# Performance work log

Hardware: AMD Instinct MI355X
Metric: run time of the kernel (lower is better)

The kernel has to match this reference:

```python
import jax, jax.numpy as jnp
import numpy as np

# Dimensions (see shape_source):
B = 256    # number of nodes (atoms)
C = 64     # num_features (channels)
Y = 16     # spherical basis size: dims of 0e+1o+2e+3o = 1+3+5+7
Z = 23     # number of symmetric-contraction paths (U.size(-1))
E = 10     # n_node_attributes (number of chemical elements, one-hot)
CORR = 3   # correlation order -> spare dims 'wxv'
CG_DENSITY = 0.1  # CG coefficient tensors are highly sparse


def setup_inputs() -> dict:
    key = jax.random.key(0)
    kU, kM, kW, kZ, kA = jax.random.split(key, 5)
    # U buffer: shape (Y,)*CORR + (Y, Z) = (16,16,16,16,23), sparse like real CG coeffs
    U = jax.random.normal(kU, (Y,) * CORR + (Y, Z), dtype=jnp.float32)
    mask = jax.random.uniform(kM, U.shape) < CG_DENSITY
    U = U * mask.astype(jnp.float32)
    # W parameter: (n_node_attributes, Z, num_features), init randn/Z as in module
    W = jax.random.normal(kW, (E, Z, C), dtype=jnp.float32) / Z
    # node embeddings: (B, C, Y)  ('bci' in the einsum)
    node_embeddings = jax.random.normal(kZ, (B, C, Y), dtype=jnp.float32)
    # node attributes: one-hot element encodings (B, E)  ('be')
    elem = jax.random.randint(kA, (B,), 0, E)
    node_attributes = jax.nn.one_hot(elem, E, dtype=jnp.float32)
    return {
        "U": U,
        "W": W,
        "node_embeddings": node_embeddings,
        "node_attributes": node_attributes,
    }


def reference(U, W, node_embeddings, node_attributes):
    # Faithful to: torch.einsum('wxvik,ekc,bci,be->bcwxv', U, W, z, a)
    # Efficient contraction order (avoids any (B,*,Y^3) intermediate except the output):
    Wb = jnp.einsum('ekc,be->bkc', W, node_attributes)        # (B, Z, C): per-node path weights
    P = jnp.einsum('bkc,bci->bcik', Wb, node_embeddings)      # (B, C, Y, Z)
    out = jnp.einsum('wxvik,bcik->bcwxv', U, P)               # (B, C, Y, Y, Y)
    return out
```

## Files before the change

kernel.cpp:

```cpp
#include <hip/hip_runtime.h>
#include <hip/hip_bf16.h>

#define B_NODES 256
#define C_FEAT  64
#define Y_DIM   16
#define Z_PATH  23
#define E_ATTR  10
#define WXV     4096
#define K_REAL  368
#define K_PAD   384
#define M_DIM   16384
#define N_DIM   4096

typedef __attribute__((ext_vector_type(8))) short bf16x8;
typedef __attribute__((ext_vector_type(8))) unsigned short u16x8;
typedef __attribute__((ext_vector_type(4))) float f32x4;

__device__ inline unsigned short f2bf(float x) {
    union { float f; unsigned u; } v; v.f = x;
    unsigned r = v.u + 0x7fffu + ((v.u >> 16) & 1u);
    return (unsigned short)(r >> 16);
}

__device__ inline void gload_lds16(const void* g, void* l) {
    __builtin_amdgcn_global_load_lds(
        (const __attribute__((address_space(1))) void*)g,
        (__attribute__((address_space(3))) void*)l,
        16, 0, 0);
}

__global__ __launch_bounds__(256) void prep_combined(
    const float* __restrict__ U, const float* __restrict__ W,
    const float* __restrict__ z, const float* __restrict__ attr,
    unsigned short* __restrict__ A, unsigned short* __restrict__ Ub)
{
    int blk = blockIdx.x;
    int tid = threadIdx.x;
    if (blk < B_NODES) {
        int b = blk;
        __shared__ float t_lds[Z_PATH * C_FEAT];
        __shared__ float z_lds[C_FEAT * Y_DIM];
        __shared__ float a_lds[E_ATTR];
        if (tid < E_ATTR) a_lds[tid] = attr[b * E_ATTR + tid];
        ((float4*)z_lds)[tid] = ((const float4*)(z + (size_t)b * 1024))[tid];
        __syncthreads();
        for (int idx = tid; idx < Z_PATH * C_FEAT; idx += 256) {
            int k = idx >> 6;
            int c = idx & 63;
            float acc = 0.f;
            #pragma unroll
            for (int e = 0; e < E_ATTR; ++e)
                acc += a_lds[e] * W[(e * Z_PATH + k) * C_FEAT + c];
            t_lds[idx] = acc;
        }
        __syncthreads();
        unsigned short* Ab = A + (size_t)b * C_FEAT * K_PAD;
        for (int u = tid; u < C_FEAT * 48; u += 256) {
            int c = u / 48;
            int g = u - c * 48;
            int j0 = g * 8;
            u16x8 pack;
            #pragma unroll
            for (int jj = 0; jj < 8; ++jj) {
                int j = j0 + jj;
                float v = 0.f;
                if (j < K_REAL) {
                    int i = j / Z_PATH;
                    int k = j - i * Z_PATH;
                    v = z_lds[c * Y_DIM + i] * t_lds[k * C_FEAT + c];
                }
                pack[jj] = f2bf(v);
            }
            *(u16x8*)&Ab[c * K_PAD + j0] = pack;
        }
    } else {
        int f = (blk - B_NODES) * 256 + tid;
        int row = f / 96;
        int q = f - row * 96;
        int j = q * 4;
        unsigned short o[4] = {0, 0, 0, 0};
        if (j < K_REAL) {
            float4 v = *(const float4*)(U + (size_t)row * K_REAL + j);
            o[0] = f2bf(v.x); o[1] = f2bf(v.y); o[2] = f2bf(v.z); o[3] = f2bf(v.w);
        }
        unsigned short* dst = Ub + (size_t)row * K_PAD + j;
        dst[0] = o[0]; dst[1] = o[1]; dst[2] = o[2]; dst[3] = o[3];
    }
}

__global__ __launch_bounds__(256) void gemm_kernel(
    const unsigned short* __restrict__ A,
    const unsigned short* __restrict__ Bt,
    float* __restrict__ C)
{
    __shared__ unsigned short sA[2][128 * 32];
    __shared__ unsigned short sB[2][128 * 32];

    int bid = blockIdx.x;
    int wg = (bid & 7) * 512 + (bid >> 3);
    int tm = wg >> 5;
    int tn = wg & 31;
    int tid = threadIdx.x;
    int lane = tid & 63;
    int w = tid >> 6;
    int wm = w >> 1, wn = w & 1;

    f32x4 acc[4][4];
    #pragma unroll
    for (int p = 0; p < 4; ++p)
        #pragma unroll
        for (int q = 0; q < 4; ++q)
            acc[p][q] = (f32x4){0.f, 0.f, 0.f, 0.f};

    const char* gA = (const char*)A + (size_t)(tm * 128) * (K_PAD * 2);
    const char* gB = (const char*)Bt + (size_t)(tn * 128) * (K_PAD * 2);
    int ch0 = w * 2;
    int lrow = lane >> 2;
    int lk16 = (lane & 3) * 16;
    int fr_row = lane & 15;
    int fr_k = (lane >> 4) * 8;

    auto stage = [&](int t, int buf) {
        #pragma unroll
        for (int s = 0; s < 2; ++s) {
            int ch = ch0 + s;
            int r = ch * 16 + lrow;
            gload_lds16(gA + (size_t)r * (K_PAD * 2) + t * 64 + lk16,
                        (char*)&sA[buf][0] + ch * 1024);
            gload_lds16(gB + (size_t)r * (K_PAD * 2) + t * 64 + lk16,
                        (char*)&sB[buf][0] + ch * 1024);
        }
    };

    stage(0, 0);
    stage(1, 1);
    __builtin_amdgcn_sched_barrier(0);
    asm volatile("s_waitcnt vmcnt(4)" ::: "memory");
    __builtin_amdgcn_sched_barrier(0);
    __builtin_amdgcn_s_barrier();

    #pragma unroll
    for (int t = 0; t < 12; ++t) {
        const int cur = t & 1;
        bf16x8 af[4], bfr[4];
        #pragma unroll
        for (int fm = 0; fm < 4; ++fm)
            af[fm] = *(const bf16x8*)&sA[cur][(wm * 64 + fm * 16 + fr_row) * 32 + fr_k];
        #pragma unroll
        for (int fn = 0; fn < 4; ++fn)
            bfr[fn] = *(const bf16x8*)&sB[cur][(wn * 64 + fn * 16 + fr_row) * 32 + fr_k];
        #pragma unroll
        for (int fm = 0; fm < 4; ++fm)
            #pragma unroll
            for (int fn = 0; fn < 4; ++fn)
                acc[fm][fn] = __builtin_amdgcn_mfma_f32_16x16x32_bf16(
                    af[fm], bfr[fn], acc[fm][fn], 0, 0, 0);
        if (t < 11) {
            __builtin_amdgcn_sched_barrier(0);
            __builtin_amdgcn_s_barrier();
            if (t < 10) stage(t + 2, cur);
            __builtin_amdgcn_sched_barrier(0);
            if (t < 10) { asm volatile("s_waitcnt vmcnt(4)" ::: "memory"); }
            else        { asm volatile("s_waitcnt vmcnt(0)" ::: "memory"); }
            __builtin_amdgcn_sched_barrier(0);
            __builtin_amdgcn_s_barrier();
            __builtin_amdgcn_sched_barrier(0);
        }
    }

    int r0 = tm * 128 + wm * 64 + (lane >> 4) * 4;
    int c0 = tn * 128 + wn * 64 + (lane & 15);
    #pragma unroll
    for (int fm = 0; fm < 4; ++fm)
        #pragma unroll
        for (int fn = 0; fn < 4; ++fn)
            #pragma unroll
            for (int reg = 0; reg < 4; ++reg)
                __builtin_nontemporal_store(acc[fm][fn][reg],
                    &C[(size_t)(r0 + fm * 16 + reg) * N_DIM + (c0 + fn * 16)]);
}

__global__ __launch_bounds__(256) void fallback_kernel(
    const float* __restrict__ U, const float* __restrict__ W,
    const float* __restrict__ z, const float* __restrict__ attr,
    float* __restrict__ out)
{
    int bc = blockIdx.x;
    int b = bc >> 6, c = bc & 63;
    int tid = threadIdx.x;
    __shared__ float zt[K_REAL];
    for (int idx = tid; idx < K_REAL; idx += 256) {
        int i = idx / Z_PATH;
        int k = idx - i * Z_PATH;
        float t = 0.f;
        #pragma unroll
        for (int e = 0; e < E_ATTR; ++e)
            t += attr[b * E_ATTR + e] * W[(e * Z_PATH + k) * C_FEAT + c];
        zt[idx] = z[((size_t)b * C_FEAT + c) * Y_DIM + i] * t;
    }
    __syncthreads();
    for (int n = tid; n < WXV; n += 256) {
        const float* Ur = U + (size_t)n * K_REAL;
        float s = 0.f;
        for (int j = 0; j < K_REAL; ++j) s += Ur[j] * zt[j];
        out[(size_t)bc * WXV + n] = s;
    }
}

extern "C" void kernel_launch(void* const* d_in, const int* in_sizes, int n_in,
                              void* d_out, int out_size, void* d_ws, size_t ws_size,
                              hipStream_t stream)
{
    const float* U    = (const float*)d_in[0];
    const float* W    = (const float*)d_in[1];
    const float* z    = (const float*)d_in[2];
    const float* attr = (const float*)d_in[3];
    float* out = (float*)d_out;

    size_t needA = (size_t)M_DIM * K_PAD * sizeof(unsigned short);
    size_t needU = (size_t)N_DIM * K_PAD * sizeof(unsigned short);
    if (ws_size >= needA + needU) {
        unsigned short* Abf = (unsigned short*)d_ws;
        unsigned short* Ubf = Abf + (size_t)M_DIM * K_PAD;
        prep_combined<<<B_NODES + (N_DIM * 96) / 256, 256, 0, stream>>>(U, W, z, attr, Abf, Ubf);
        gemm_kernel<<<4096, 256, 0, stream>>>(Abf, Ubf, out);
    } else {
        fallback_kernel<<<M_DIM, 256, 0, stream>>>(U, W, z, attr, out);
    }
}
```

Before: 104.0 us.

## Replace 128x128 GEMM with 256x256 tile, 8 waves, swizzled LDS and split pipeline

The bf16 MFMA GEMM moves from 128x128 tiles with 4 waves and K-step 32 to 256x256 tiles with 8 waves and K-step 64. LDS rows are XOR-swizzled to avoid bank conflicts, and the A and B staging is staggered across four quarter-steps so the next tile's loads interleave with the MFMA blocks. Raising wave priority around the MFMAs is meant to keep the matrix units busy. The larger tiles cut redundant global and LDS traffic per output, at the cost of more registers, 128 KB of LDS per block and far fewer workgroups (1024).

```diff
diff --git a/kernel.cpp b/kernel.cpp
--- a/kernel.cpp
+++ b/kernel.cpp
@@ -11,6 +11,7 @@
 #define K_PAD   384
 #define M_DIM   16384
 #define N_DIM   4096
+#define ROWB    (K_PAD * 2)
 
 typedef __attribute__((ext_vector_type(8))) short bf16x8;
 typedef __attribute__((ext_vector_type(8))) unsigned short u16x8;
@@ -88,96 +89,142 @@
     }
 }
 
-__global__ __launch_bounds__(256) void gemm_kernel(
+__global__ __launch_bounds__(512, 2) void gemm256(
     const unsigned short* __restrict__ A,
     const unsigned short* __restrict__ Bt,
     float* __restrict__ C)
 {
-    __shared__ unsigned short sA[2][128 * 32];
-    __shared__ unsigned short sB[2][128 * 32];
+    __shared__ __align__(16) unsigned short sA[2][256 * 64];
+    __shared__ __align__(16) unsigned short sB[2][256 * 64];
 
     int bid = blockIdx.x;
-    int wg = (bid & 7) * 512 + (bid >> 3);
-    int tm = wg >> 5;
-    int tn = wg & 31;
+    int wg = (bid & 7) * 128 + (bid >> 3);
+    int tm = wg >> 4;
+    int tn = wg & 15;
     int tid = threadIdx.x;
     int lane = tid & 63;
     int w = tid >> 6;
-    int wm = w >> 1, wn = w & 1;
-
-    f32x4 acc[4][4];
+    int wm = w >> 2;
+    int wn = w & 3;
+
+    const char* gA = (const char*)A + (size_t)(tm * 256) * ROWB;
+    const char* gB = (const char*)Bt + (size_t)(tn * 256) * ROWB;
+
+    int chunk0 = w * 2;
+    int srow = lane >> 3;
+    int gslot = (lane & 7) ^ srow;
+
+    auto stage = [&](const char* gbase, unsigned short* lds, int t, int h) {
+        #pragma unroll
+        for (int L = 0; L < 2; ++L) {
+            int chunk = chunk0 + L;
+            gload_lds16(gbase + (size_t)(h * 128 + chunk * 8 + srow) * ROWB
+                              + t * 128 + gslot * 16,
+                        (char*)lds + h * 16384 + chunk * 1024);
+        }
+    };
+
+    int frow = lane & 15;
+    int fsb = lane >> 4;
+    int fxor = lane & 7;
+
+    auto rdA = [&](int b, int frag, int ks) -> bf16x8 {
+        int row = wm * 128 + frag * 16 + frow;
+        int slot = (ks * 4 + fsb) ^ fxor;
+        return *(const bf16x8*)((const char*)&sA[b][0] + row * 128 + slot * 16);
+    };
+    auto rdB = [&](int b, int frag, int ks) -> bf16x8 {
+        int row = wn * 64 + frag * 16 + frow;
+        int slot = (ks * 4 + fsb) ^ fxor;
+        return *(const bf16x8*)((const char*)&sB[b][0] + row * 128 + slot * 16);
+    };
+
+    f32x4 acc[8][4];
     #pragma unroll
-    for (int p = 0; p < 4; ++p)
+    for (int p = 0; p < 8; ++p)
         #pragma unroll
         for (int q = 0; q < 4; ++q)
             acc[p][q] = (f32x4){0.f, 0.f, 0.f, 0.f};
 
-    const char* gA = (const char*)A + (size_t)(tm * 128) * (K_PAD * 2);
-    const char* gB = (const char*)Bt + (size_t)(tn * 128) * (K_PAD * 2);
-    int ch0 = w * 2;
-    int lrow = lane >> 2;
-    int lk16 = (lane & 3) * 16;
-    int fr_row = lane & 15;
-    int fr_k = (lane >> 4) * 8;
-
-    auto stage = [&](int t, int buf) {
-        #pragma unroll
-        for (int s = 0; s < 2; ++s) {
-            int ch = ch0 + s;
-            int r = ch * 16 + lrow;
-            gload_lds16(gA + (size_t)r * (K_PAD * 2) + t * 64 + lk16,
-                        (char*)&sA[buf][0] + ch * 1024);
-            gload_lds16(gB + (size_t)r * (K_PAD * 2) + t * 64 + lk16,
-                        (char*)&sB[buf][0] + ch * 1024);
-        }
-    };
-
-    stage(0, 0);
-    stage(1, 1);
+    bf16x8 aq[4][2], bq[2][2][2];
+
+    stage(gA, &sA[0][0], 0, 0); stage(gA, &sA[0][0], 0, 1);
+    stage(gB, &sB[0][0], 0, 0); stage(gB, &sB[0][0], 0, 1);
+    stage(gB, &sB[1][0], 1, 0); stage(gB, &sB[1][0], 1, 1);
     __builtin_amdgcn_sched_barrier(0);
     asm volatile("s_waitcnt vmcnt(4)" ::: "memory");
     __builtin_amdgcn_sched_barrier(0);
     __builtin_amdgcn_s_barrier();
 
     #pragma unroll
-    for (int t = 0; t < 12; ++t) {
-        const int cur = t & 1;
-        bf16x8 af[4], bfr[4];
-        #pragma unroll
-        for (int fm = 0; fm < 4; ++fm)
-            af[fm] = *(const bf16x8*)&sA[cur][(wm * 64 + fm * 16 + fr_row) * 32 + fr_k];
-        #pragma unroll
-        for (int fn = 0; fn < 4; ++fn)
-            bfr[fn] = *(const bf16x8*)&sB[cur][(wn * 64 + fn * 16 + fr_row) * 32 + fr_k];
-        #pragma unroll
-        for (int fm = 0; fm < 4; ++fm)
-            #pragma unroll
-            for (int fn = 0; fn < 4; ++fn)
-                acc[fm][fn] = __builtin_amdgcn_mfma_f32_16x16x32_bf16(
-                    af[fm], bfr[fn], acc[fm][fn], 0, 0, 0);
-        if (t < 11) {
+    for (int t = 0; t < 6; ++t) {
+        const int b = t & 1;
+        #pragma unroll
+        for (int q = 0; q < 4; ++q) {
+            const int mh = q >> 1;
+            const int nh = q & 1;
+            if (q == 0) {
+                #pragma unroll
+                for (int f = 0; f < 4; ++f)
+                    #pragma unroll
+                    for (int ks = 0; ks < 2; ++ks)
+                        aq[f][ks] = rdA(b, f, ks);
+                #pragma unroll
+                for (int g = 0; g < 2; ++g)
+                    #pragma unroll
+                    for (int ks = 0; ks < 2; ++ks)
+                        bq[0][g][ks] = rdB(b, g, ks);
+            } else if (q == 1) {
+                #pragma unroll
+                for (int g = 0; g < 2; ++g)
+                    #pragma unroll
+                    for (int ks = 0; ks < 2; ++ks)
+                        bq[1][g][ks] = rdB(b, 2 + g, ks);
+            } else if (q == 2) {
+                #pragma unroll
+                for (int f = 0; f < 4; ++f)
+                    #pragma unroll
+                    for (int ks = 0; ks < 2; ++ks)
+                        aq[f][ks] = rdA(b, 4 + f, ks);
+            }
+            if (q == 0 && t + 1 < 6) stage(gA, &sA[(t + 1) & 1][0], t + 1, 0);
+            if (q == 1 && t + 1 < 6) stage(gA, &sA[(t + 1) & 1][0], t + 1, 1);
+            if (q == 2 && t + 2 < 6) stage(gB, &sB[b][0], t + 2, 0);
+            if (q == 3 && t + 2 < 6) stage(gB, &sB[b][0], t + 2, 1);
             __builtin_amdgcn_sched_barrier(0);
             __builtin_amdgcn_s_barrier();
-            if (t < 10) stage(t + 2, cur);
+            asm volatile("s_waitcnt lgkmcnt(0)" ::: "memory");
             __builtin_amdgcn_sched_barrier(0);
-            if (t < 10) { asm volatile("s_waitcnt vmcnt(4)" ::: "memory"); }
-            else        { asm volatile("s_waitcnt vmcnt(0)" ::: "memory"); }
+            __builtin_amdgcn_s_setprio(1);
+            #pragma unroll
+            for (int f = 0; f < 4; ++f)
+                #pragma unroll
+                for (int g = 0; g < 2; ++g)
+                    #pragma unroll
+                    for (int ks = 0; ks < 2; ++ks)
+                        acc[mh * 4 + f][nh * 2 + g] = __builtin_amdgcn_mfma_f32_16x16x32_bf16(
+                            aq[f][ks], bq[nh][g][ks], acc[mh * 4 + f][nh * 2 + g], 0, 0, 0);
+            __builtin_amdgcn_s_setprio(0);
             __builtin_amdgcn_sched_barrier(0);
-            __builtin_amdgcn_s_barrier();
-            __builtin_amdgcn_sched_barrier(0);
-        }
-    }
-
-    int r0 = tm * 128 + wm * 64 + (lane >> 4) * 4;
-    int c0 = tn * 128 + wn * 64 + (lane & 15);
+            if (q == 3) {
+                if (t < 4)       asm volatile("s_waitcnt vmcnt(4)" ::: "memory");
+                else if (t == 4) asm volatile("s_waitcnt vmcnt(0)" ::: "memory");
+                __builtin_amdgcn_sched_barrier(0);
+            }
+            if (!(t == 5 && q == 3)) __builtin_amdgcn_s_barrier();
+        }
+    }
+
+    float* Cw = C + (size_t)(tm * 256 + wm * 128 + (lane >> 4) * 4) * N_DIM
+                  + tn * 256 + wn * 64 + (lane & 15);
     #pragma unroll
-    for (int fm = 0; fm < 4; ++fm)
-        #pragma unroll
-        for (int fn = 0; fn < 4; ++fn)
-            #pragma unroll
-            for (int reg = 0; reg < 4; ++reg)
+    for (int fm = 0; fm < 8; ++fm)
+        #pragma unroll
+        for (int reg = 0; reg < 4; ++reg)
+            #pragma unroll
+            for (int fn = 0; fn < 4; ++fn)
                 __builtin_nontemporal_store(acc[fm][fn][reg],
-                    &C[(size_t)(r0 + fm * 16 + reg) * N_DIM + (c0 + fn * 16)]);
+                    Cw + (size_t)(fm * 16 + reg) * N_DIM + fn * 16);
 }
 
 __global__ __launch_bounds__(256) void fallback_kernel(
@@ -223,7 +270,7 @@
         unsigned short* Abf = (unsigned short*)d_ws;
         unsigned short* Ubf = Abf + (size_t)M_DIM * K_PAD;
         prep_combined<<<B_NODES + (N_DIM * 96) / 256, 256, 0, stream>>>(U, W, z, attr, Abf, Ubf);
-        gemm_kernel<<<4096, 256, 0, stream>>>(Abf, Ubf, out);
+        gemm256<<<1024, 512, 0, stream>>>(Abf, Ubf, out);
     } else {
         fallback_kernel<<<M_DIM, 256, 0, stream>>>(U, W, z, attr, out);
     }
```

Result: slower. 122.3 us (+17.6%).

## Triple-buffer GEMM LDS staging with XOR swizzle and one barrier per step

Applied to the files above, without the earlier changes.

Moves the bf16 GEMM from double to triple LDS buffering. The next tile's global→LDS load is issued before the current tile's MFMAs, and only one workgroup barrier is needed per K step instead of two. The LDS layout gains an XOR swizzle on 16-byte k-chunks to reduce bank conflicts on fragment reads, and the block-to-tile mapping is regrouped into 16x8 tile chunks per XCD slot. It also vectorizes the padded U bf16 store in the prep kernel. The cost is extra LDS per workgroup, which may lower occupancy, and the kernel likely stays bound by the large fp32 output writes.

```diff
diff --git a/kernel.cpp b/kernel.cpp
--- a/kernel.cpp
+++ b/kernel.cpp
@@ -11,9 +11,11 @@
 #define K_PAD   384
 #define M_DIM   16384
 #define N_DIM   4096
+#define ROWB    (K_PAD * 2)
 
 typedef __attribute__((ext_vector_type(8))) short bf16x8;
 typedef __attribute__((ext_vector_type(8))) unsigned short u16x8;
+typedef __attribute__((ext_vector_type(4))) unsigned short u16x4;
 typedef __attribute__((ext_vector_type(4))) float f32x4;
 
 __device__ inline unsigned short f2bf(float x) {
@@ -78,13 +80,12 @@
         int row = f / 96;
         int q = f - row * 96;
         int j = q * 4;
-        unsigned short o[4] = {0, 0, 0, 0};
+        u16x4 o = (u16x4){0, 0, 0, 0};
         if (j < K_REAL) {
             float4 v = *(const float4*)(U + (size_t)row * K_REAL + j);
             o[0] = f2bf(v.x); o[1] = f2bf(v.y); o[2] = f2bf(v.z); o[3] = f2bf(v.w);
         }
-        unsigned short* dst = Ub + (size_t)row * K_PAD + j;
-        dst[0] = o[0]; dst[1] = o[1]; dst[2] = o[2]; dst[3] = o[3];
+        *(u16x4*)&Ub[(size_t)row * K_PAD + j] = o;
     }
 }
 
@@ -93,13 +94,17 @@
     const unsigned short* __restrict__ Bt,
     float* __restrict__ C)
 {
-    __shared__ unsigned short sA[2][128 * 32];
-    __shared__ unsigned short sB[2][128 * 32];
+    __shared__ __align__(16) unsigned short sA[3][128 * 32];
+    __shared__ __align__(16) unsigned short sB[3][128 * 32];
 
     int bid = blockIdx.x;
-    int wg = (bid & 7) * 512 + (bid >> 3);
-    int tm = wg >> 5;
-    int tn = wg & 31;
+    int x = bid & 7;
+    int r = bid >> 3;
+    int chunk = r >> 7;
+    int i = r & 127;
+    int tm = x * 16 + (i >> 3);
+    int tn = chunk * 8 + (i & 7);
+
     int tid = threadIdx.x;
     int lane = tid & 63;
     int w = tid >> 6;
@@ -112,25 +117,26 @@
         for (int q = 0; q < 4; ++q)
             acc[p][q] = (f32x4){0.f, 0.f, 0.f, 0.f};
 
-    const char* gA = (const char*)A + (size_t)(tm * 128) * (K_PAD * 2);
-    const char* gB = (const char*)Bt + (size_t)(tn * 128) * (K_PAD * 2);
+    const char* gA = (const char*)A + (size_t)(tm * 128) * ROWB;
+    const char* gB = (const char*)Bt + (size_t)(tn * 128) * ROWB;
     int ch0 = w * 2;
     int lrow = lane >> 2;
-    int lk16 = (lane & 3) * 16;
-    int fr_row = lane & 15;
-    int fr_k = (lane >> 4) * 8;
+    int lk16 = ((lane & 3) ^ ((lane >> 3) & 3)) * 16;
 
     auto stage = [&](int t, int buf) {
         #pragma unroll
         for (int s = 0; s < 2; ++s) {
             int ch = ch0 + s;
-            int r = ch * 16 + lrow;
-            gload_lds16(gA + (size_t)r * (K_PAD * 2) + t * 64 + lk16,
+            int rr = ch * 16 + lrow;
+            gload_lds16(gA + (size_t)rr * ROWB + t * 64 + lk16,
                         (char*)&sA[buf][0] + ch * 1024);
-            gload_lds16(gB + (size_t)r * (K_PAD * 2) + t * 64 + lk16,
+            gload_lds16(gB + (size_t)rr * ROWB + t * 64 + lk16,
                         (char*)&sB[buf][0] + ch * 1024);
         }
     };
+
+    int fr_row = lane & 15;
+    int fslot = ((lane >> 4) ^ ((fr_row >> 1) & 3)) * 16;
 
     stage(0, 0);
     stage(1, 1);
@@ -141,31 +147,28 @@
 
     #pragma unroll
     for (int t = 0; t < 12; ++t) {
-        const int cur = t & 1;
+        const int cur = t % 3;
+        if (t < 10) stage(t + 2, (t + 2) % 3);
         bf16x8 af[4], bfr[4];
         #pragma unroll
         for (int fm = 0; fm < 4; ++fm)
-            af[fm] = *(const bf16x8*)&sA[cur][(wm * 64 + fm * 16 + fr_row) * 32 + fr_k];
+            af[fm] = *(const bf16x8*)((const char*)&sA[cur][0]
+                     + (wm * 64 + fm * 16 + fr_row) * 64 + fslot);
         #pragma unroll
         for (int fn = 0; fn < 4; ++fn)
-            bfr[fn] = *(const bf16x8*)&sB[cur][(wn * 64 + fn * 16 + fr_row) * 32 + fr_k];
+            bfr[fn] = *(const bf16x8*)((const char*)&sB[cur][0]
+                     + (wn * 64 + fn * 16 + fr_row) * 64 + fslot);
         #pragma unroll
         for (int fm = 0; fm < 4; ++fm)
             #pragma unroll
             for (int fn = 0; fn < 4; ++fn)
                 acc[fm][fn] = __builtin_amdgcn_mfma_f32_16x16x32_bf16(
                     af[fm], bfr[fn], acc[fm][fn], 0, 0, 0);
-        if (t < 11) {
-            __builtin_amdgcn_sched_barrier(0);
-            __builtin_amdgcn_s_barrier();
-            if (t < 10) stage(t + 2, cur);
-            __builtin_amdgcn_sched_barrier(0);
-            if (t < 10) { asm volatile("s_waitcnt vmcnt(4)" ::: "memory"); }
-            else        { asm volatile("s_waitcnt vmcnt(0)" ::: "memory"); }
-            __builtin_amdgcn_sched_barrier(0);
-            __builtin_amdgcn_s_barrier();
-            __builtin_amdgcn_sched_barrier(0);
-        }
+        __builtin_amdgcn_sched_barrier(0);
+        if (t < 10)       { asm volatile("s_waitcnt vmcnt(4)" ::: "memory"); }
+        else if (t == 10) { asm volatile("s_waitcnt vmcnt(0)" ::: "memory"); }
+        __builtin_amdgcn_sched_barrier(0);
+        if (t < 11) __builtin_amdgcn_s_barrier();
     }
 
     int r0 = tm * 128 + wm * 64 + (lane >> 4) * 4;
```

After: 120.3 us. 15.7% more time.

## Pre-swizzle operands into MFMA fragment layout and load directly to registers

Applied to the files above, without the earlier changes.

The prep kernel now writes A and U in bf16 into a fragment-major layout, grouped by 16 rows and 32-wide k steps, so each lane's bf16x8 MFMA operand is contiguous. The GEMM drops the LDS double buffer, barriers and global_load_lds staging. Each wave loads its fragments straight from global memory into registers with a two-stage ping-pong. This removes LDS traffic and synchronisation, but fragments are no longer shared through LDS, so each wave re-fetches data from global/L2 that its sibling waves also use.

```diff
diff --git a/kernel.cpp b/kernel.cpp
--- a/kernel.cpp
+++ b/kernel.cpp
@@ -11,6 +11,8 @@
 #define K_PAD   384
 #define M_DIM   16384
 #define N_DIM   4096
+#define GRP_STRIDE 6144
+#define W_STRIDE   512
 
 typedef __attribute__((ext_vector_type(8))) short bf16x8;
 typedef __attribute__((ext_vector_type(8))) unsigned short u16x8;
@@ -22,17 +24,10 @@
     return (unsigned short)(r >> 16);
 }
 
-__device__ inline void gload_lds16(const void* g, void* l) {
-    __builtin_amdgcn_global_load_lds(
-        (const __attribute__((address_space(1))) void*)g,
-        (__attribute__((address_space(3))) void*)l,
-        16, 0, 0);
-}
-
 __global__ __launch_bounds__(256) void prep_combined(
     const float* __restrict__ U, const float* __restrict__ W,
     const float* __restrict__ z, const float* __restrict__ attr,
-    unsigned short* __restrict__ A, unsigned short* __restrict__ Ub)
+    unsigned short* __restrict__ At, unsigned short* __restrict__ Bt)
 {
     int blk = blockIdx.x;
     int tid = threadIdx.x;
@@ -54,7 +49,6 @@
             t_lds[idx] = acc;
         }
         __syncthreads();
-        unsigned short* Ab = A + (size_t)b * C_FEAT * K_PAD;
         for (int u = tid; u < C_FEAT * 48; u += 256) {
             int c = u / 48;
             int g = u - c * 48;
@@ -71,39 +65,44 @@
                 }
                 pack[jj] = f2bf(v);
             }
-            *(u16x8*)&Ab[c * K_PAD + j0] = pack;
+            int rg = b * 4 + (c >> 4);
+            size_t off = (size_t)rg * GRP_STRIDE + (g >> 2) * W_STRIDE
+                       + ((g & 3) * 16 + (c & 15)) * 8;
+            *(u16x8*)&At[off] = pack;
         }
     } else {
         int f = (blk - B_NODES) * 256 + tid;
-        int row = f / 96;
-        int q = f - row * 96;
-        int j = q * 4;
-        unsigned short o[4] = {0, 0, 0, 0};
-        if (j < K_REAL) {
-            float4 v = *(const float4*)(U + (size_t)row * K_REAL + j);
-            o[0] = f2bf(v.x); o[1] = f2bf(v.y); o[2] = f2bf(v.z); o[3] = f2bf(v.w);
-        }
-        unsigned short* dst = Ub + (size_t)row * K_PAD + j;
-        dst[0] = o[0]; dst[1] = o[1]; dst[2] = o[2]; dst[3] = o[3];
+        int row = f / 48;
+        int g = f - row * 48;
+        int j0 = g * 8;
+        u16x8 pack;
+        #pragma unroll
+        for (int jj = 0; jj < 8; ++jj) {
+            int j = j0 + jj;
+            pack[jj] = (j < K_REAL) ? f2bf(U[(size_t)row * K_REAL + j]) : (unsigned short)0;
+        }
+        size_t off = (size_t)(row >> 4) * GRP_STRIDE + (g >> 2) * W_STRIDE
+                   + ((g & 3) * 16 + (row & 15)) * 8;
+        *(u16x8*)&Bt[off] = pack;
     }
 }
 
 __global__ __launch_bounds__(256) void gemm_kernel(
-    const unsigned short* __restrict__ A,
+    const unsigned short* __restrict__ At,
     const unsigned short* __restrict__ Bt,
     float* __restrict__ C)
 {
-    __shared__ unsigned short sA[2][128 * 32];
-    __shared__ unsigned short sB[2][128 * 32];
-
     int bid = blockIdx.x;
     int wg = (bid & 7) * 512 + (bid >> 3);
     int tm = wg >> 5;
     int tn = wg & 31;
     int tid = threadIdx.x;
     int lane = tid & 63;
-    int w = tid >> 6;
-    int wm = w >> 1, wn = w & 1;
+    int w4 = tid >> 6;
+    int wm = w4 >> 1, wn = w4 & 1;
+
+    const unsigned short* pA = At + (size_t)(tm * 8 + wm * 4) * GRP_STRIDE + lane * 8;
+    const unsigned short* pB = Bt + (size_t)(tn * 8 + wn * 4) * GRP_STRIDE + lane * 8;
 
     f32x4 acc[4][4];
     #pragma unroll
@@ -112,61 +111,32 @@
         for (int q = 0; q < 4; ++q)
             acc[p][q] = (f32x4){0.f, 0.f, 0.f, 0.f};
 
-    const char* gA = (const char*)A + (size_t)(tm * 128) * (K_PAD * 2);
-    const char* gB = (const char*)Bt + (size_t)(tn * 128) * (K_PAD * 2);
-    int ch0 = w * 2;
-    int lrow = lane >> 2;
-    int lk16 = (lane & 3) * 16;
-    int fr_row = lane & 15;
-    int fr_k = (lane >> 4) * 8;
-
-    auto stage = [&](int t, int buf) {
-        #pragma unroll
-        for (int s = 0; s < 2; ++s) {
-            int ch = ch0 + s;
-            int r = ch * 16 + lrow;
-            gload_lds16(gA + (size_t)r * (K_PAD * 2) + t * 64 + lk16,
-                        (char*)&sA[buf][0] + ch * 1024);
-            gload_lds16(gB + (size_t)r * (K_PAD * 2) + t * 64 + lk16,
-                        (char*)&sB[buf][0] + ch * 1024);
-        }
-    };
-
-    stage(0, 0);
-    stage(1, 1);
-    __builtin_amdgcn_sched_barrier(0);
-    asm volatile("s_waitcnt vmcnt(4)" ::: "memory");
-    __builtin_amdgcn_sched_barrier(0);
-    __builtin_amdgcn_s_barrier();
-
+    bf16x8 a0[4], b0[4], a1[4], b1[4];
+
+    #define LOADF(av, bv, w)                                                     \
+        _Pragma("unroll")                                                        \
+        for (int f = 0; f < 4; ++f) {                                            \
+            av[f] = *(const bf16x8*)(pA + f * GRP_STRIDE + (w) * W_STRIDE);      \
+            bv[f] = *(const bf16x8*)(pB + f * GRP_STRIDE + (w) * W_STRIDE);      \
+        }
+    #define MFMAF(av, bv)                                                        \
+        _Pragma("unroll")                                                        \
+        for (int fm = 0; fm < 4; ++fm)                                           \
+            _Pragma("unroll")                                                    \
+            for (int fn = 0; fn < 4; ++fn)                                       \
+                acc[fm][fn] = __builtin_amdgcn_mfma_f32_16x16x32_bf16(           \
+                    av[fm], bv[fn], acc[fm][fn], 0, 0, 0);
+
+    LOADF(a0, b0, 0)
     #pragma unroll
-    for (int t = 0; t < 12; ++t) {
-        const int cur = t & 1;
-        bf16x8 af[4], bfr[4];
-        #pragma unroll
-        for (int fm = 0; fm < 4; ++fm)
-            af[fm] = *(const bf16x8*)&sA[cur][(wm * 64 + fm * 16 + fr_row) * 32 + fr_k];
-        #pragma unroll
-        for (int fn = 0; fn < 4; ++fn)
-            bfr[fn] = *(const bf16x8*)&sB[cur][(wn * 64 + fn * 16 + fr_row) * 32 + fr_k];
-        #pragma unroll
-        for (int fm = 0; fm < 4; ++fm)
-            #pragma unroll
-            for (int fn = 0; fn < 4; ++fn)
-                acc[fm][fn] = __builtin_amdgcn_mfma_f32_16x16x32_bf16(
-                    af[fm], bfr[fn], acc[fm][fn], 0, 0, 0);
-        if (t < 11) {
-            __builtin_amdgcn_sched_barrier(0);
-            __builtin_amdgcn_s_barrier();
-            if (t < 10) stage(t + 2, cur);
-            __builtin_amdgcn_sched_barrier(0);
-            if (t < 10) { asm volatile("s_waitcnt vmcnt(4)" ::: "memory"); }
-            else        { asm volatile("s_waitcnt vmcnt(0)" ::: "memory"); }
-            __builtin_amdgcn_sched_barrier(0);
-            __builtin_amdgcn_s_barrier();
-            __builtin_amdgcn_sched_barrier(0);
-        }
-    }
+    for (int w = 0; w < 12; w += 2) {
+        if (w + 1 < 12) LOADF(a1, b1, w + 1)
+        MFMAF(a0, b0)
+        if (w + 2 < 12) LOADF(a0, b0, w + 2)
+        MFMAF(a1, b1)
+    }
+    #undef LOADF
+    #undef MFMAF
 
     int r0 = tm * 128 + wm * 64 + (lane >> 4) * 4;
     int c0 = tn * 128 + wn * 64 + (lane & 15);
@@ -220,10 +190,10 @@
     size_t needA = (size_t)M_DIM * K_PAD * sizeof(unsigned short);
     size_t needU = (size_t)N_DIM * K_PAD * sizeof(unsigned short);
     if (ws_size >= needA + needU) {
-        unsigned short* Abf = (unsigned short*)d_ws;
-        unsigned short* Ubf = Abf + (size_t)M_DIM * K_PAD;
-        prep_combined<<<B_NODES + (N_DIM * 96) / 256, 256, 0, stream>>>(U, W, z, attr, Abf, Ubf);
-        gemm_kernel<<<4096, 256, 0, stream>>>(Abf, Ubf, out);
+        unsigned short* At = (unsigned short*)d_ws;
+        unsigned short* Bt = At + (size_t)M_DIM * K_PAD;
+        prep_combined<<<B_NODES + (N_DIM * 48) / 256, 256, 0, stream>>>(U, W, z, attr, At, Bt);
+        gemm_kernel<<<4096, 256, 0, stream>>>(At, Bt, out);
     } else {
         fallback_kernel<<<M_DIM, 256, 0, stream>>>(U, W, z, attr, out);
     }
```

After: 121.3 us. 16.7% more time.
